# Kernel tuning notes

Measured on AMD Instinct MI355X. Metric: run time of the kernel, lower is better.

Reference implementation:

```python
import jax, jax.numpy as jnp
import numpy as np

N = 2048      # num_nodes
B = 16        # batch
D_IN = 2      # input_dim per node
UNITS = 64    # rnn_units
F = D_IN + UNITS   # concat feature size = 66
M = 3         # num_matrices = (1 support + 1 adp hop)*K(=1) + 1 identity
E = N * 16    # sparse support edges (avg degree 16)


def _spmm(rows, cols, vals, x):
    # sparse support @ x, x: (N, K); equivalent of torch.sparse.mm
    return jax.ops.segment_sum(vals[:, None] * x[cols], rows, num_segments=N)


def _gconv(inputs, state, W, support_rows, support_cols, support_vals, adp):
    # inputs: (B, N*D_IN), state: (B, N*units) -> out: (B, N*out_dim)
    x = jnp.concatenate([inputs.reshape(B, N, -1), state.reshape(B, N, -1)], axis=2)  # (B,N,F)
    f = x.shape[2]
    x0 = x.transpose(1, 2, 0).reshape(N, f * B)                # (N, F*B)
    # diffusion step 1 over the single random_walk support
    x1 = _spmm(support_rows, support_cols, support_vals, x0)   # (N, F*B)
    # adaptive adjacency, k_hop=1 -> adp_lst = [adp], applied to x0
    x_temp = x0.reshape(N, f, B).transpose(2, 0, 1)            # (B,N,F)
    x2 = jnp.einsum('bnm,bmf->bnf', adp, x_temp)               # (B,N,F)
    x2 = x2.transpose(1, 2, 0).reshape(N, f * B)
    xs = jnp.stack([x0, x1, x2], axis=0)                       # (M,N,F*B)
    xs = xs.reshape(M, N, f, B).transpose(3, 1, 2, 0).reshape(B * N, f * M)
    out = xs @ W                                               # (B*N, out_dim)  (no bias: source never adds it)
    return out.reshape(B, N * W.shape[1])


def setup_inputs() -> dict:
    key = jax.random.key(0)
    ks = jax.random.split(key, 8)
    inputs = jax.random.normal(ks[0], (B, N * D_IN), dtype=jnp.float32)
    hx = jax.random.normal(ks[1], (B, N * UNITS), dtype=jnp.float32)
    adp = jax.random.uniform(ks[2], (B, N, N), dtype=jnp.float32) / N  # ~row-stochastic adaptive adj
    support_rows = jax.random.randint(ks[3], (E,), 0, N, dtype=jnp.int32)
    support_cols = jax.random.randint(ks[4], (E,), 0, N, dtype=jnp.int32)
    support_vals = jax.random.uniform(ks[5], (E,), dtype=jnp.float32) / 16.0
    W_ru = jax.random.normal(ks[6], (F * M, 2 * UNITS), dtype=jnp.float32) * 0.05
    W_c = jax.random.normal(ks[7], (F * M, UNITS), dtype=jnp.float32) * 0.05
    return dict(inputs=inputs, hx=hx, adp=adp, support_rows=support_rows,
                support_cols=support_cols, support_vals=support_vals,
                W_ru=W_ru, W_c=W_c, time_axis=0)


def reference(inputs, hx, adp, support_rows, support_cols, support_vals, W_ru, W_c, time_axis):
    # GRU with graph convolution gates (use_gc_for_ru=True, activation=tanh)
    ru = jax.nn.sigmoid(_gconv(inputs, hx, W_ru, support_rows, support_cols, support_vals, adp))
    ru = ru.reshape(B, N, 2 * UNITS)
    r = ru[..., :UNITS].reshape(B, N * UNITS)
    u = ru[..., UNITS:].reshape(B, N * UNITS)
    c = jnp.tanh(_gconv(inputs, r * hx, W_c, support_rows, support_cols, support_vals, adp))
    return u * hx + (1.0 - u) * c
```

## Files before the change

kernel.cpp:

```cpp
#include <hip/hip_runtime.h>
#include <cstdint>
#include <cstddef>

#define DN 2048
#define DB 16
#define DE 32768
#define FPAD 96

typedef __bf16 bf16x8 __attribute__((ext_vector_type(8)));
typedef float f32x4 __attribute__((ext_vector_type(4)));

__global__ __launch_bounds__(256) void prep_kernel(
    const float* __restrict__ inputs, const float* __restrict__ hx,
    const float* __restrict__ Wru, const float* __restrict__ Wc,
    __bf16* __restrict__ xcat1, __bf16* __restrict__ xcat2,
    __bf16* __restrict__ wtru, __bf16* __restrict__ wtc,
    int* __restrict__ cnt) {
  int idx = blockIdx.x * 256 + threadIdx.x;
  const int T1 = DB * DN * FPAD;
  if (idx < 2 * T1) {
    int which = idx >= T1 ? 1 : 0;
    int i = idx - which * T1;
    int f = i % FPAD;
    int bn = i / FPAD;
    int n = bn & (DN - 1);
    int b = bn >> 11;
    __bf16 v = (__bf16)0.0f;
    if (f < 2) v = (__bf16)inputs[(b << 12) + n * 2 + f];
    else if (f < 66 && !which) v = (__bf16)hx[((size_t)b << 17) + (n << 6) + (f - 2)];
    if (which) xcat2[i] = v; else xcat1[i] = v;
  } else {
    int j = idx - 2 * T1;
    if (j < 384 * FPAD) {
      int k = j % FPAD, o = j / FPAD;
      wtru[j] = (k < 66) ? (__bf16)Wru[(k * 3 + (o >> 7)) * 128 + (o & 127)] : (__bf16)0.0f;
    } else {
      j -= 384 * FPAD;
      if (j < 192 * FPAD) {
        int k = j % FPAD, o = j / FPAD;
        wtc[j] = (k < 66) ? (__bf16)Wc[(k * 3 + (o >> 6)) * 64 + (o & 63)] : (__bf16)0.0f;
      } else {
        j -= 192 * FPAD;
        if (j < DN) cnt[j] = 0;
      }
    }
  }
}

__global__ __launch_bounds__(512) void csr_count(const int* __restrict__ rows,
                                                 int* __restrict__ cnt) {
  int e = blockIdx.x * 512 + threadIdx.x;
  atomicAdd(&cnt[rows[e]], 1);
}

__global__ __launch_bounds__(1024) void csr_scan(const int* __restrict__ cnt,
                                                 int* __restrict__ csr_ptr,
                                                 int* __restrict__ off) {
  __shared__ int sa[DN];
  __shared__ int sb[DN];
  int t = threadIdx.x;
  int c0 = cnt[t], c1 = cnt[t + 1024];
  sa[t] = c0; sa[t + 1024] = c1;
  __syncthreads();
  int* src = sa; int* dst = sb;
  for (int o = 1; o < DN; o <<= 1) {
    for (int i = t; i < DN; i += 1024) {
      int v = src[i];
      if (i >= o) v += src[i - o];
      dst[i] = v;
    }
    __syncthreads();
    int* tmp = src; src = dst; dst = tmp;
  }
  int e0 = src[t] - c0;
  int e1 = src[t + 1024] - c1;
  csr_ptr[t] = e0; csr_ptr[t + 1024] = e1;
  off[t] = e0; off[t + 1024] = e1;
  if (t == 0) csr_ptr[DN] = DE;
}

__global__ __launch_bounds__(512) void csr_scatter(
    const int* __restrict__ rows, const int* __restrict__ cols,
    const float* __restrict__ vals, int* __restrict__ off,
    int* __restrict__ csr_col, float* __restrict__ csr_val) {
  int e = blockIdx.x * 512 + threadIdx.x;
  int r = rows[e];
  int p = atomicAdd(&off[r], 1);
  csr_col[p] = cols[e];
  csr_val[p] = vals[e];
}

template <int OD>
__global__ __launch_bounds__(256) void small_gemm(
    const __bf16* __restrict__ A, const __bf16* __restrict__ Bt,
    float* __restrict__ Y0, __bf16* __restrict__ y1b, __bf16* __restrict__ y2b) {
  __shared__ __attribute__((aligned(16))) __bf16 As[128 * 104];
  __shared__ __attribute__((aligned(16))) __bf16 Bs[64 * 104];
  int tid = threadIdx.x;
  int wave = tid >> 6, lane = tid & 63;
  int lrow = lane & 15, quad = lane >> 4;
  int r0 = blockIdx.x * 128;
  int c0 = blockIdx.y * 64;
  const uint4* gA = (const uint4*)(A + (size_t)r0 * FPAD);
  const uint4* gB = (const uint4*)(Bt + (size_t)c0 * FPAD);
  uint4* sA = (uint4*)As;
  uint4* sB = (uint4*)Bs;
#pragma unroll
  for (int i = 0; i < 6; ++i) {
    int s = i * 256 + tid;
    int r = s / 12, c4 = s % 12;
    sA[r * 13 + c4] = gA[r * 12 + c4];
  }
#pragma unroll
  for (int i = 0; i < 3; ++i) {
    int s = i * 256 + tid;
    int r = s / 12, c4 = s % 12;
    sB[r * 13 + c4] = gB[r * 12 + c4];
  }
  __syncthreads();
  int wm = wave >> 1, wn = wave & 1;
  f32x4 acc[4][2];
#pragma unroll
  for (int mt = 0; mt < 4; ++mt)
#pragma unroll
    for (int nt = 0; nt < 2; ++nt) acc[mt][nt] = (f32x4){0.f, 0.f, 0.f, 0.f};
#pragma unroll
  for (int kk = 0; kk < 3; ++kk) {
    bf16x8 af[4], bv[2];
#pragma unroll
    for (int mt = 0; mt < 4; ++mt)
      af[mt] = *(const bf16x8*)(As + (wm * 64 + mt * 16 + lrow) * 104 + kk * 32 + quad * 8);
#pragma unroll
    for (int nt = 0; nt < 2; ++nt)
      bv[nt] = *(const bf16x8*)(Bs + (wn * 32 + nt * 16 + lrow) * 104 + kk * 32 + quad * 8);
#pragma unroll
    for (int mt = 0; mt < 4; ++mt)
#pragma unroll
      for (int nt = 0; nt < 2; ++nt)
        acc[mt][nt] = __builtin_amdgcn_mfma_f32_16x16x32_bf16(af[mt], bv[nt], acc[mt][nt], 0, 0, 0);
  }
#pragma unroll
  for (int mt = 0; mt < 4; ++mt)
#pragma unroll
    for (int nt = 0; nt < 2; ++nt)
#pragma unroll
      for (int r = 0; r < 4; ++r) {
        int row = r0 + wm * 64 + mt * 16 + quad * 4 + r;
        int col = c0 + wn * 32 + nt * 16 + lrow;
        float v = acc[mt][nt][r];
        int g = col >> ((OD == 128) ? 7 : 6);
        int oo = col & (OD - 1);
        size_t oi = (size_t)row * OD + oo;
        if (g == 0) Y0[oi] = v;
        else if (g == 1) y1b[oi] = (__bf16)v;
        else y2b[oi] = (__bf16)v;
      }
}

template <int OD>
__global__ __launch_bounds__(256) void gather_pre(
    float* __restrict__ Y0, const __bf16* __restrict__ y1b,
    const int* __restrict__ csr_ptr, const int* __restrict__ csr_col,
    const float* __restrict__ csr_val) {
  constexpr int SH = (OD == 128) ? 7 : 6;
  int idx = blockIdx.x * 256 + threadIdx.x;
  int o = idx & (OD - 1);
  int bn = idx >> SH;
  int n = bn & (DN - 1);
  int b = bn >> 11;
  float acc = Y0[idx];
  int e1 = csr_ptr[n + 1];
  const __bf16* yb = y1b + ((size_t)b << 11) * OD;
  for (int e = csr_ptr[n]; e < e1; ++e)
    acc += csr_val[e] * (float)yb[(size_t)csr_col[e] * OD + o];
  Y0[idx] = acc;
}

template <int OD>
__global__ void transpose_y2(const __bf16* __restrict__ y2b, __bf16* __restrict__ y2t) {
  __shared__ __bf16 tile[32][33];
  int b = blockIdx.z;
  int mb = blockIdx.x * 32, ob = blockIdx.y * 32;
  int tx = threadIdx.x, ty = threadIdx.y;
#pragma unroll
  for (int i = 0; i < 4; ++i)
    tile[ty + i * 8][tx] = y2b[(size_t)(b * DN + mb + ty + i * 8) * OD + ob + tx];
  __syncthreads();
#pragma unroll
  for (int i = 0; i < 4; ++i)
    y2t[(size_t)(b * OD + ob + ty + i * 8) * DN + mb + tx] = tile[tx][ty + i * 8];
}

template <int OD, bool IS_RU>
__global__ __launch_bounds__(256) void adp_gemm(
    const float* __restrict__ adp, const __bf16* __restrict__ y2t,
    const float* __restrict__ pre, const float* __restrict__ hx,
    float* __restrict__ u_buf, __bf16* __restrict__ xcat2,
    float* __restrict__ outp) {
  constexpr int BM = 64;
  constexpr int BN = OD;
  constexpr int MT = 2;
  constexpr int NT = OD / 32;
  constexpr int LDK = 72;
  constexpr int NA = (BM * 8) / 256;
  constexpr int NB = (BN * 8) / 256;
  __shared__ __attribute__((aligned(16))) __bf16 As[BM * LDK];
  __shared__ __attribute__((aligned(16))) __bf16 Bs[BN * LDK];
  int tid = threadIdx.x;
  int wave = tid >> 6, lane = tid & 63;
  int lrow = lane & 15, quad = lane >> 4;
  int b = blockIdx.y;
  int row0 = blockIdx.x * BM;
  const float* Ab = adp + ((size_t)b * DN + row0) * DN;
  const __bf16* Bb = y2t + (size_t)b * OD * DN;
  int wm = wave >> 1, wn = wave & 1;
  f32x4 acc[MT][NT];
#pragma unroll
  for (int mt = 0; mt < MT; ++mt)
#pragma unroll
    for (int nt = 0; nt < NT; ++nt) acc[mt][nt] = (f32x4){0.f, 0.f, 0.f, 0.f};

  f32x4 ra[NA][2];
  uint4 rb[NB];
#pragma unroll
  for (int i = 0; i < NA; ++i) {
    int s = i * 256 + tid, r = s >> 3, cc = s & 7;
    const float* p = Ab + (size_t)r * DN + cc * 8;
    ra[i][0] = *(const f32x4*)p;
    ra[i][1] = *(const f32x4*)(p + 4);
  }
#pragma unroll
  for (int i = 0; i < NB; ++i) {
    int s = i * 256 + tid, r = s >> 3, cc = s & 7;
    rb[i] = *(const uint4*)(Bb + (size_t)r * DN + cc * 8);
  }

  for (int c = 0; c < DN / 64; ++c) {
    __syncthreads();
#pragma unroll
    for (int i = 0; i < NA; ++i) {
      int s = i * 256 + tid, r = s >> 3, cc = s & 7;
      bf16x8 cv;
#pragma unroll
      for (int j = 0; j < 4; ++j) cv[j] = (__bf16)ra[i][0][j];
#pragma unroll
      for (int j = 0; j < 4; ++j) cv[4 + j] = (__bf16)ra[i][1][j];
      *(bf16x8*)(As + r * LDK + cc * 8) = cv;
    }
#pragma unroll
    for (int i = 0; i < NB; ++i) {
      int s = i * 256 + tid, r = s >> 3, cc = s & 7;
      *(uint4*)(Bs + r * LDK + cc * 8) = rb[i];
    }
    __syncthreads();
    if (c < DN / 64 - 1) {
      int k0 = (c + 1) * 64;
#pragma unroll
      for (int i = 0; i < NA; ++i) {
        int s = i * 256 + tid, r = s >> 3, cc = s & 7;
        const float* p = Ab + (size_t)r * DN + k0 + cc * 8;
        ra[i][0] = *(const f32x4*)p;
        ra[i][1] = *(const f32x4*)(p + 4);
      }
#pragma unroll
      for (int i = 0; i < NB; ++i) {
        int s = i * 256 + tid, r = s >> 3, cc = s & 7;
        rb[i] = *(const uint4*)(Bb + (size_t)r * DN + k0 + cc * 8);
      }
    }
#pragma unroll
    for (int kk = 0; kk < 2; ++kk) {
      bf16x8 af[MT], bv[NT];
#pragma unroll
      for (int mt = 0; mt < MT; ++mt) {
        int r = wm * 32 + mt * 16 + lrow;
        af[mt] = *(const bf16x8*)(As + r * LDK + (kk * 4 + quad) * 8);
      }
#pragma unroll
      for (int nt = 0; nt < NT; ++nt) {
        int r = wn * (NT * 16) + nt * 16 + lrow;
        bv[nt] = *(const bf16x8*)(Bs + r * LDK + (kk * 4 + quad) * 8);
      }
#pragma unroll
      for (int mt = 0; mt < MT; ++mt)
#pragma unroll
        for (int nt = 0; nt < NT; ++nt)
          acc[mt][nt] = __builtin_amdgcn_mfma_f32_16x16x32_bf16(af[mt], bv[nt], acc[mt][nt], 0, 0, 0);
    }
  }
#pragma unroll
  for (int mt = 0; mt < MT; ++mt)
#pragma unroll
    for (int nt = 0; nt < NT; ++nt)
#pragma unroll
      for (int r = 0; r < 4; ++r) {
        int n = row0 + wm * 32 + mt * 16 + quad * 4 + r;
        int o = wn * (NT * 16) + nt * 16 + lrow;
        float g = acc[mt][nt][r] + pre[((size_t)b * DN + n) * OD + o];
        if (IS_RU) {
          float s = 1.f / (1.f + __expf(-g));
          if (o < 64) {
            float hxv = hx[((size_t)b << 17) + n * 64 + o];
            xcat2[((size_t)b * DN + n) * FPAD + 2 + o] = (__bf16)(s * hxv);
          } else {
            u_buf[((size_t)b * DN + n) * 64 + (o - 64)] = s;
          }
        } else {
          float cval = 1.f - 2.f / (__expf(2.f * g) + 1.f);
          float u = u_buf[((size_t)b * DN + n) * 64 + o];
          float hxv = hx[((size_t)b << 17) + n * 64 + o];
          outp[((size_t)b << 17) + n * 64 + o] = u * hxv + (1.f - u) * cval;
        }
      }
}

extern "C" void kernel_launch(void* const* d_in, const int* in_sizes, int n_in,
                              void* d_out, int out_size, void* d_ws, size_t ws_size,
                              hipStream_t stream) {
  const float* inputs = (const float*)d_in[0];
  const float* hx     = (const float*)d_in[1];
  const float* adp    = (const float*)d_in[2];
  const int* srows    = (const int*)d_in[3];
  const int* scols    = (const int*)d_in[4];
  const float* svals  = (const float*)d_in[5];
  const float* Wru    = (const float*)d_in[6];
  const float* Wc     = (const float*)d_in[7];
  float* outp = (float*)d_out;

  char* w = (char*)d_ws;
  auto carve = [&](size_t bytes) -> char* {
    char* p = w;
    w += (bytes + 255) & ~(size_t)255;
    return p;
  };
  int*    csr_ptr = (int*)   carve((DN + 1) * sizeof(int));
  int*    csr_col = (int*)   carve(DE * sizeof(int));
  float*  csr_val = (float*) carve(DE * sizeof(float));
  int*    cnt     = (int*)   carve(DN * sizeof(int));
  int*    off     = (int*)   carve(DN * sizeof(int));
  __bf16* xcat1   = (__bf16*)carve((size_t)DB * DN * FPAD * 2);
  __bf16* xcat2   = (__bf16*)carve((size_t)DB * DN * FPAD * 2);
  __bf16* wtru    = (__bf16*)carve(384 * FPAD * 2);
  __bf16* wtc     = (__bf16*)carve(192 * FPAD * 2);
  float*  Y0      = (float*) carve((size_t)DB * DN * 128 * 4);
  __bf16* y1b     = (__bf16*)carve((size_t)DB * DN * 128 * 2);
  __bf16* y2b     = (__bf16*)carve((size_t)DB * DN * 128 * 2);
  __bf16* y2t     = (__bf16*)carve((size_t)DB * DN * 128 * 2);
  float*  u_buf   = (float*) carve((size_t)DB * DN * 64 * 4);
  (void)ws_size; (void)in_sizes; (void)n_in; (void)out_size;

  prep_kernel<<<24800, 256, 0, stream>>>(inputs, hx, Wru, Wc, xcat1, xcat2,
                                         wtru, wtc, cnt);
  csr_count<<<64, 512, 0, stream>>>(srows, cnt);
  csr_scan<<<1, 1024, 0, stream>>>(cnt, csr_ptr, off);
  csr_scatter<<<64, 512, 0, stream>>>(srows, scols, svals, off, csr_col, csr_val);

  small_gemm<128><<<dim3(256, 6), 256, 0, stream>>>(xcat1, wtru, Y0, y1b, y2b);
  gather_pre<128><<<16384, 256, 0, stream>>>(Y0, y1b, csr_ptr, csr_col, csr_val);
  transpose_y2<128><<<dim3(64, 4, 16), dim3(32, 8), 0, stream>>>(y2b, y2t);
  adp_gemm<128, true><<<dim3(32, 16), 256, 0, stream>>>(
      adp, y2t, Y0, hx, u_buf, xcat2, outp);

  small_gemm<64><<<dim3(256, 3), 256, 0, stream>>>(xcat2, wtc, Y0, y1b, y2b);
  gather_pre<64><<<8192, 256, 0, stream>>>(Y0, y1b, csr_ptr, csr_col, csr_val);
  transpose_y2<64><<<dim3(64, 2, 16), dim3(32, 8), 0, stream>>>(y2b, y2t);
  adp_gemm<64, false><<<dim3(32, 16), 256, 0, stream>>>(
      adp, y2t, Y0, hx, u_buf, xcat2, outp);
}
```

Before: 722.0 us.

## Restructure adp_gemm with smaller row tiles, direct B loads, and double-buffered A

Halves the row tile to 32 so 1024 blocks are launched instead of 512, which gives more parallelism across CUs for the memory-bound fp32 adp stream. B fragments (y2t) are now read straight from global or L2 into registers instead of being staged in shared memory. A is double-buffered in LDS, so each 64-wide k-chunk needs one barrier instead of two. A swizzled block index spreads batches across XCDs, and launch bounds request 4 blocks per CU. The cost is that each block re-reads its B slice from L2 with no LDS reuse, and there is a risk of register pressure.

```diff
diff --git a/kernel.cpp b/kernel.cpp
--- a/kernel.cpp
+++ b/kernel.cpp
@@ -192,126 +192,122 @@
 }
 
 template <int OD, bool IS_RU>
-__global__ __launch_bounds__(256) void adp_gemm(
+__global__ __launch_bounds__(256, 4) void adp_gemm(
     const float* __restrict__ adp, const __bf16* __restrict__ y2t,
     const float* __restrict__ pre, const float* __restrict__ hx,
     float* __restrict__ u_buf, __bf16* __restrict__ xcat2,
     float* __restrict__ outp) {
-  constexpr int BM = 64;
-  constexpr int BN = OD;
-  constexpr int MT = 2;
+  constexpr int BM = 32;
   constexpr int NT = OD / 32;
   constexpr int LDK = 72;
-  constexpr int NA = (BM * 8) / 256;
-  constexpr int NB = (BN * 8) / 256;
-  __shared__ __attribute__((aligned(16))) __bf16 As[BM * LDK];
-  __shared__ __attribute__((aligned(16))) __bf16 Bs[BN * LDK];
+  constexpr int ASZ = BM * LDK;
+  __shared__ __attribute__((aligned(16))) __bf16 As[2 * ASZ];
   int tid = threadIdx.x;
   int wave = tid >> 6, lane = tid & 63;
   int lrow = lane & 15, quad = lane >> 4;
-  int b = blockIdx.y;
-  int row0 = blockIdx.x * BM;
+  int hw = blockIdx.x;
+  int swz = (hw & 7) * 128 + (hw >> 3);
+  int b = swz >> 6;
+  int row0 = (swz & 63) * BM;
   const float* Ab = adp + ((size_t)b * DN + row0) * DN;
-  const __bf16* Bb = y2t + (size_t)b * OD * DN;
+  const __bf16* Bb = y2t + (size_t)b * OD * (size_t)DN;
   int wm = wave >> 1, wn = wave & 1;
-  f32x4 acc[MT][NT];
-#pragma unroll
-  for (int mt = 0; mt < MT; ++mt)
-#pragma unroll
-    for (int nt = 0; nt < NT; ++nt) acc[mt][nt] = (f32x4){0.f, 0.f, 0.f, 0.f};
-
-  f32x4 ra[NA][2];
-  uint4 rb[NB];
-#pragma unroll
-  for (int i = 0; i < NA; ++i) {
-    int s = i * 256 + tid, r = s >> 3, cc = s & 7;
-    const float* p = Ab + (size_t)r * DN + cc * 8;
-    ra[i][0] = *(const f32x4*)p;
-    ra[i][1] = *(const f32x4*)(p + 4);
-  }
-#pragma unroll
-  for (int i = 0; i < NB; ++i) {
-    int s = i * 256 + tid, r = s >> 3, cc = s & 7;
-    rb[i] = *(const uint4*)(Bb + (size_t)r * DN + cc * 8);
-  }
-
-  for (int c = 0; c < DN / 64; ++c) {
-    __syncthreads();
-#pragma unroll
-    for (int i = 0; i < NA; ++i) {
-      int s = i * 256 + tid, r = s >> 3, cc = s & 7;
+  f32x4 acc[NT];
+#pragma unroll
+  for (int nt = 0; nt < NT; ++nt) acc[nt] = (f32x4){0.f, 0.f, 0.f, 0.f};
+
+  int ar = tid >> 3;
+  int ac = (tid & 7) * 8;
+  const float* ap = Ab + (size_t)ar * DN + ac;
+  int awofs = ar * LDK + ac;
+  int arofs = (wm * 16 + lrow) * LDK;
+
+  f32x4 raA0 = *(const f32x4*)ap;
+  f32x4 raA1 = *(const f32x4*)(ap + 4);
+  f32x4 raB0 = *(const f32x4*)(ap + 64);
+  f32x4 raB1 = *(const f32x4*)(ap + 68);
+
+#pragma unroll 1
+  for (int c2 = 0; c2 < DN / 128; ++c2) {
+    {
+      int c = 2 * c2;
       bf16x8 cv;
 #pragma unroll
-      for (int j = 0; j < 4; ++j) cv[j] = (__bf16)ra[i][0][j];
-#pragma unroll
-      for (int j = 0; j < 4; ++j) cv[4 + j] = (__bf16)ra[i][1][j];
-      *(bf16x8*)(As + r * LDK + cc * 8) = cv;
-    }
-#pragma unroll
-    for (int i = 0; i < NB; ++i) {
-      int s = i * 256 + tid, r = s >> 3, cc = s & 7;
-      *(uint4*)(Bs + r * LDK + cc * 8) = rb[i];
-    }
-    __syncthreads();
-    if (c < DN / 64 - 1) {
-      int k0 = (c + 1) * 64;
-#pragma unroll
-      for (int i = 0; i < NA; ++i) {
-        int s = i * 256 + tid, r = s >> 3, cc = s & 7;
-        const float* p = Ab + (size_t)r * DN + k0 + cc * 8;
-        ra[i][0] = *(const f32x4*)p;
-        ra[i][1] = *(const f32x4*)(p + 4);
-      }
-#pragma unroll
-      for (int i = 0; i < NB; ++i) {
-        int s = i * 256 + tid, r = s >> 3, cc = s & 7;
-        rb[i] = *(const uint4*)(Bb + (size_t)r * DN + k0 + cc * 8);
-      }
-    }
-#pragma unroll
-    for (int kk = 0; kk < 2; ++kk) {
-      bf16x8 af[MT], bv[NT];
-#pragma unroll
-      for (int mt = 0; mt < MT; ++mt) {
-        int r = wm * 32 + mt * 16 + lrow;
-        af[mt] = *(const bf16x8*)(As + r * LDK + (kk * 4 + quad) * 8);
-      }
-#pragma unroll
-      for (int nt = 0; nt < NT; ++nt) {
-        int r = wn * (NT * 16) + nt * 16 + lrow;
-        bv[nt] = *(const bf16x8*)(Bs + r * LDK + (kk * 4 + quad) * 8);
-      }
-#pragma unroll
-      for (int mt = 0; mt < MT; ++mt)
+      for (int j = 0; j < 4; ++j) { cv[j] = (__bf16)raA0[j]; cv[4 + j] = (__bf16)raA1[j]; }
+      *(bf16x8*)(As + awofs) = cv;
+      bf16x8 bv[2][NT];
+#pragma unroll
+      for (int kk = 0; kk < 2; ++kk)
+#pragma unroll
+        for (int nt = 0; nt < NT; ++nt) {
+          int rb = wn * (NT * 16) + nt * 16 + lrow;
+          bv[kk][nt] = *(const bf16x8*)(Bb + (size_t)rb * DN + c * 64 + (kk * 4 + quad) * 8);
+        }
+      if (c + 2 < DN / 64) {
+        const float* pn = ap + (c + 2) * 64;
+        raA0 = *(const f32x4*)pn;
+        raA1 = *(const f32x4*)(pn + 4);
+      }
+      __syncthreads();
+#pragma unroll
+      for (int kk = 0; kk < 2; ++kk) {
+        bf16x8 af = *(const bf16x8*)(As + arofs + (kk * 4 + quad) * 8);
 #pragma unroll
         for (int nt = 0; nt < NT; ++nt)
-          acc[mt][nt] = __builtin_amdgcn_mfma_f32_16x16x32_bf16(af[mt], bv[nt], acc[mt][nt], 0, 0, 0);
-    }
-  }
-#pragma unroll
-  for (int mt = 0; mt < MT; ++mt)
-#pragma unroll
-    for (int nt = 0; nt < NT; ++nt)
-#pragma unroll
-      for (int r = 0; r < 4; ++r) {
-        int n = row0 + wm * 32 + mt * 16 + quad * 4 + r;
-        int o = wn * (NT * 16) + nt * 16 + lrow;
-        float g = acc[mt][nt][r] + pre[((size_t)b * DN + n) * OD + o];
-        if (IS_RU) {
-          float s = 1.f / (1.f + __expf(-g));
-          if (o < 64) {
-            float hxv = hx[((size_t)b << 17) + n * 64 + o];
-            xcat2[((size_t)b * DN + n) * FPAD + 2 + o] = (__bf16)(s * hxv);
-          } else {
-            u_buf[((size_t)b * DN + n) * 64 + (o - 64)] = s;
-          }
+          acc[nt] = __builtin_amdgcn_mfma_f32_16x16x32_bf16(af, bv[kk][nt], acc[nt], 0, 0, 0);
+      }
+    }
+    {
+      int c = 2 * c2 + 1;
+      bf16x8 cv;
+#pragma unroll
+      for (int j = 0; j < 4; ++j) { cv[j] = (__bf16)raB0[j]; cv[4 + j] = (__bf16)raB1[j]; }
+      *(bf16x8*)(As + ASZ + awofs) = cv;
+      bf16x8 bv[2][NT];
+#pragma unroll
+      for (int kk = 0; kk < 2; ++kk)
+#pragma unroll
+        for (int nt = 0; nt < NT; ++nt) {
+          int rb = wn * (NT * 16) + nt * 16 + lrow;
+          bv[kk][nt] = *(const bf16x8*)(Bb + (size_t)rb * DN + c * 64 + (kk * 4 + quad) * 8);
+        }
+      if (c + 2 < DN / 64) {
+        const float* pn = ap + (c + 2) * 64;
+        raB0 = *(const f32x4*)pn;
+        raB1 = *(const f32x4*)(pn + 4);
+      }
+      __syncthreads();
+#pragma unroll
+      for (int kk = 0; kk < 2; ++kk) {
+        bf16x8 af = *(const bf16x8*)(As + ASZ + arofs + (kk * 4 + quad) * 8);
+#pragma unroll
+        for (int nt = 0; nt < NT; ++nt)
+          acc[nt] = __builtin_amdgcn_mfma_f32_16x16x32_bf16(af, bv[kk][nt], acc[nt], 0, 0, 0);
+      }
+    }
+  }
+#pragma unroll
+  for (int nt = 0; nt < NT; ++nt)
+#pragma unroll
+    for (int r = 0; r < 4; ++r) {
+      int n = row0 + wm * 16 + quad * 4 + r;
+      int o = wn * (NT * 16) + nt * 16 + lrow;
+      float g = acc[nt][r] + pre[((size_t)b * DN + n) * OD + o];
+      if (IS_RU) {
+        float s = 1.f / (1.f + __expf(-g));
+        if (o < 64) {
+          float hxv = hx[((size_t)b << 17) + n * 64 + o];
+          xcat2[((size_t)b * DN + n) * FPAD + 2 + o] = (__bf16)(s * hxv);
         } else {
-          float cval = 1.f - 2.f / (__expf(2.f * g) + 1.f);
-          float u = u_buf[((size_t)b * DN + n) * 64 + o];
-          float hxv = hx[((size_t)b << 17) + n * 64 + o];
-          outp[((size_t)b << 17) + n * 64 + o] = u * hxv + (1.f - u) * cval;
+          u_buf[((size_t)b * DN + n) * 64 + (o - 64)] = s;
         }
-      }
+      } else {
+        float cval = 1.f - 2.f / (__expf(2.f * g) + 1.f);
+        float u = u_buf[((size_t)b * DN + n) * 64 + o];
+        float hxv = hx[((size_t)b << 17) + n * 64 + o];
+        outp[((size_t)b << 17) + n * 64 + o] = u * hxv + (1.f - u) * cval;
+      }
+    }
 }
 
 extern "C" void kernel_launch(void* const* d_in, const int* in_sizes, int n_in,
@@ -358,12 +354,12 @@
   small_gemm<128><<<dim3(256, 6), 256, 0, stream>>>(xcat1, wtru, Y0, y1b, y2b);
   gather_pre<128><<<16384, 256, 0, stream>>>(Y0, y1b, csr_ptr, csr_col, csr_val);
   transpose_y2<128><<<dim3(64, 4, 16), dim3(32, 8), 0, stream>>>(y2b, y2t);
-  adp_gemm<128, true><<<dim3(32, 16), 256, 0, stream>>>(
+  adp_gemm<128, true><<<1024, 256, 0, stream>>>(
       adp, y2t, Y0, hx, u_buf, xcat2, outp);
 
   small_gemm<64><<<dim3(256, 3), 256, 0, stream>>>(xcat2, wtc, Y0, y1b, y2b);
   gather_pre<64><<<8192, 256, 0, stream>>>(Y0, y1b, csr_ptr, csr_col, csr_val);
   transpose_y2<64><<<dim3(64, 2, 16), dim3(32, 8), 0, stream>>>(y2b, y2t);
-  adp_gemm<64, false><<<dim3(32, 16), 256, 0, stream>>>(
+  adp_gemm<64, false><<<1024, 256, 0, stream>>>(
       adp, y2t, Y0, hx, u_buf, xcat2, outp);
 }
```

Measured after the change: 732.0 us. About the same (+1.4%).
